# Kernel optimization log

Hardware: AMD Instinct MI355X
Metric: run time of the kernel (lower is better)

Reference implementation:

```python
import jax, jax.numpy as jnp
import numpy as np

B, M, D = 16, 100000, 128
OUT = 128  # out_features; in_features = 2*D


def setup_inputs() -> dict:
    key = jax.random.key(0)
    k1, k2, k3, k4 = jax.random.split(key, 4)
    s1 = 1.0 / np.sqrt(2 * D)  # ~ torch Linear default init scale
    s2 = 1.0 / np.sqrt(OUT)
    return {
        "xx_anchor": jax.random.normal(k1, (B, D), dtype=jnp.float32),
        "input": jax.random.normal(k2, (M, D), dtype=jnp.float32),
        "adj": jnp.zeros((1, 1), dtype=jnp.float32),  # densified then unused in forward math
        "W1": jax.random.normal(k3, (OUT, 2 * D), dtype=jnp.float32) * s1,
        "W2": jax.random.normal(k4, (1, OUT), dtype=jnp.float32) * s2,
    }


def reference(xx_anchor, input, adj, W1, W2):
    d = input.shape[1]
    # concat(q_vec, input) @ W1.T  ==  q @ W1[:, :d].T  +  input @ W1[:, d:].T
    # (avoids materializing the [B, m, 2d] concat tensor; same math)
    anchor_part = xx_anchor @ W1[:, :d].T          # [B, out]
    node_part = input @ W1[:, d:].T                # [m, out]
    h = jax.nn.relu(anchor_part[:, None, :] + node_part[None, :, :])  # [B, m, out]
    scores = jnp.einsum('bmo,o->bm', h, W2[0])     # linear2 -> [B, m]
    atten = jax.nn.softmax(scores, axis=1)          # softmax over node dim
    v_vec = jnp.einsum('bm,md->bd', atten, input)   # weighted sum pooling
    return v_vec
```

## Files before the change

### kernel.cpp

```cpp
#include <hip/hip_runtime.h>
#include <hip/hip_bf16.h>
#include <math.h>


typedef __attribute__((ext_vector_type(8))) short bf16x8;
typedef __attribute__((ext_vector_type(4))) float f32x4;

__device__ __forceinline__ short f2bs(float f) {
    __hip_bfloat16 h = __float2bfloat16(f);
    return *reinterpret_cast<short*>(&h);
}
__device__ __forceinline__ float bs2f(ushort u) {
    union { unsigned int i; float f; } v; v.i = ((unsigned)u) << 16; return v.f;
}

__global__ __launch_bounds__(256) void kA(const float* __restrict__ W1,
                                          const float* __restrict__ xx,
                                          ushort* __restrict__ w1b,
                                          float* __restrict__ A) {
    const int bi = blockIdx.x, t = threadIdx.x;
    if (bi < 64) {
        int idx = bi * 256 + t;
        int o = idx >> 7, d = idx & 127;
        w1b[idx] = (ushort)f2bs(W1[o * 256 + 128 + d]);
        return;
    }
    __shared__ float xxs[16 * 132];
    __shared__ float w1s[16 * 132];
    const int og0 = (bi - 64) * 16;
#pragma unroll
    for (int i = 0; i < 2; ++i) {
        int idx = t + 256 * i;
        int r = idx >> 5, c4 = (idx & 31) << 2;
        *(float4*)&xxs[r * 132 + c4] = *(const float4*)&xx[r * 128 + c4];
        *(float4*)&w1s[r * 132 + c4] = *(const float4*)&W1[(og0 + r) * 256 + c4];
    }
    __syncthreads();
    const int ol = t >> 4, b = t & 15;
    float acc = 0.f;
#pragma unroll
    for (int d4 = 0; d4 < 32; ++d4) {
        float4 xv = *(float4*)&xxs[b * 132 + d4 * 4];
        float4 wv = *(float4*)&w1s[ol * 132 + d4 * 4];
        acc += xv.x * wv.x + xv.y * wv.y + xv.z * wv.z + xv.w * wv.w;
    }
    A[b * 128 + og0 + ol] = acc;
}

__global__ __launch_bounds__(256, 4) void kB(
    const float* __restrict__ in, const ushort* __restrict__ w1b,
    const float* __restrict__ W2, const float* __restrict__ A,
    float* __restrict__ lsum_g, ushort* __restrict__ pacc, int M) {
    __shared__ ushort ins[64 * 136];
    __shared__ float As[16 * 128];
    __shared__ ushort pb[16 * 72];

    const int tid = threadIdx.x, bid = blockIdx.x;
    const int m0 = bid * 64;
    const int w = tid >> 6, lane = tid & 63;
    const int c = lane & 15, q = lane >> 4;
    const int lim = (M - m0 < 64) ? (M - m0) : 64;

#pragma unroll
    for (int i = 0; i < 8; ++i) {
        int idx = tid + 256 * i;
        int r = idx >> 5, c4 = (idx & 31) << 2;
        float4 v = make_float4(0.f, 0.f, 0.f, 0.f);
        if (r < lim) v = *(const float4*)&in[(size_t)(m0 + r) * 128 + c4];
        ushort4 u;
        u.x = (ushort)f2bs(v.x); u.y = (ushort)f2bs(v.y);
        u.z = (ushort)f2bs(v.z); u.w = (ushort)f2bs(v.w);
        *(ushort4*)&ins[r * 136 + c4] = u;
    }
#pragma unroll
    for (int i = 0; i < 8; ++i) {
        int idx = tid + 256 * i;
        As[idx] = A[idx];
    }
    __syncthreads();

    const ushort* mrow = &ins[(w * 16 + c) * 136];
    f32x4 acc[8];
#pragma unroll
    for (int ot = 0; ot < 8; ++ot) acc[ot] = (f32x4){0.f, 0.f, 0.f, 0.f};
#pragma unroll
    for (int kb = 0; kb < 4; ++kb) {
        bf16x8 bv_in = *(const bf16x8*)(mrow + kb * 32 + q * 8);
#pragma unroll
        for (int ot = 0; ot < 8; ++ot) {
            bf16x8 av_w1 = *(const bf16x8*)(w1b + (ot * 16 + c) * 128 + kb * 32 + q * 8);
            acc[ot] = __builtin_amdgcn_mfma_f32_16x16x32_bf16(av_w1, bv_in, acc[ot], 0, 0, 0);
        }
    }

    f32x4 w2q[8];
#pragma unroll
    for (int ot = 0; ot < 8; ++ot)
        w2q[ot] = *(const f32x4*)&W2[ot * 16 + q * 4];

    const bool mvalid = (w * 16 + c) < lim;
#pragma unroll
    for (int b = 0; b < 16; ++b) {
        float s0 = 0.f, s1 = 0.f, s2 = 0.f, s3 = 0.f;
#pragma unroll
        for (int ot = 0; ot < 8; ++ot) {
            f32x4 aq = *(f32x4*)&As[b * 128 + ot * 16 + q * 4];
            s0 += fmaxf(acc[ot][0] + aq[0], 0.f) * w2q[ot][0];
            s1 += fmaxf(acc[ot][1] + aq[1], 0.f) * w2q[ot][1];
            s2 += fmaxf(acc[ot][2] + aq[2], 0.f) * w2q[ot][2];
            s3 += fmaxf(acc[ot][3] + aq[3], 0.f) * w2q[ot][3];
        }
        float sacc = (s0 + s1) + (s2 + s3);
        sacc += __shfl_xor(sacc, 16, 64);
        sacc += __shfl_xor(sacc, 32, 64);
        if (q == (b & 3)) {
            float p = mvalid ? __expf(sacc) : 0.f;
            pb[b * 72 + w * 16 + c] = (ushort)f2bs(p);
        }
    }
    __syncthreads();

    f32x4 pd[2];
    pd[0] = (f32x4){0.f, 0.f, 0.f, 0.f};
    pd[1] = (f32x4){0.f, 0.f, 0.f, 0.f};
#pragma unroll
    for (int s = 0; s < 2; ++s) {
        bf16x8 pf = *(const bf16x8*)(pb + c * 72 + s * 32 + q * 8);
#pragma unroll
        for (int t = 0; t < 2; ++t) {
            const int dloc = w * 32 + t * 16 + c;
            bf16x8 bf;
#pragma unroll
            for (int j = 0; j < 8; ++j)
                bf[j] = (short)ins[(s * 32 + q * 8 + j) * 136 + dloc];
            pd[t] = __builtin_amdgcn_mfma_f32_16x16x32_bf16(pf, bf, pd[t], 0, 0, 0);
        }
    }
#pragma unroll
    for (int t = 0; t < 2; ++t)
#pragma unroll
        for (int r = 0; r < 4; ++r)
            pacc[((size_t)bid * 16 + q * 4 + r) * 128 + w * 32 + t * 16 + c] =
                (ushort)f2bs(pd[t][r]);

    {
        const int b = tid >> 4, jj = tid & 15;
        const ushort* pr = &pb[b * 72 + jj * 4];
        float part = bs2f(pr[0]) + bs2f(pr[1]) + bs2f(pr[2]) + bs2f(pr[3]);
#pragma unroll
        for (int off = 1; off < 16; off <<= 1) part += __shfl_xor(part, off, 64);
        if (jj == 0) lsum_g[bid * 16 + b] = part;
    }
}

__global__ __launch_bounds__(256) void kC1(
    const float* __restrict__ lsum_g, const ushort* __restrict__ pacc,
    float* __restrict__ pacc2, float* __restrict__ lsum2, int nb) {
    const int b = blockIdx.x >> 4, s = blockIdx.x & 15;
    const int t = threadIdx.x;
    __shared__ float reda[2 * 128];
    __shared__ float redl[2];
    const int cs = (nb + 15) >> 4;
    const int blk0 = s * cs;
    int blk1 = blk0 + cs; if (blk1 > nb) blk1 = nb;
    const int dd = t & 127, h = t >> 7;
    float ac = 0.f, ls = 0.f;
    for (int blk = blk0 + h; blk < blk1; blk += 2) {
        ac += bs2f(pacc[((size_t)blk * 16 + b) * 128 + dd]);
        ls += lsum_g[blk * 16 + b];
    }
    reda[h * 128 + dd] = ac;
    if (dd == 0) redl[h] = ls;
    __syncthreads();
    if (h == 0) {
        pacc2[((size_t)s * 16 + b) * 128 + dd] = reda[dd] + reda[128 + dd];
        if (dd == 0) lsum2[s * 16 + b] = redl[0] + redl[1];
    }
}

__global__ void kFin(const float* __restrict__ pacc2, const float* __restrict__ lsum2,
                     float* __restrict__ out) {
    const int b = blockIdx.x, t = threadIdx.x;
    float ac = 0.f, ls = 0.f;
#pragma unroll
    for (int s = 0; s < 16; ++s) {
        ac += pacc2[((size_t)s * 16 + b) * 128 + t];
        ls += lsum2[s * 16 + b];
    }
    out[b * 128 + t] = ac / ls;
}

extern "C" void kernel_launch(void* const* d_in, const int* in_sizes, int n_in,
                              void* d_out, int out_size, void* d_ws, size_t ws_size,
                              hipStream_t stream) {
    const float* xx = (const float*)d_in[0];
    const float* in = (const float*)d_in[1];
    const float* W1 = (const float*)d_in[3];
    const float* W2 = (const float*)d_in[4];
    float* out = (float*)d_out;

    const int M = in_sizes[1] / 128;
    const int nb = (M + 63) / 64;

    float* ws = (float*)d_ws;
    float* A      = ws;
    float* lsum_g = A + 2048;
    float* pacc2  = lsum_g + (size_t)nb * 16;
    float* lsum2  = pacc2 + 256 * 128;
    ushort* w1b   = (ushort*)(lsum2 + 256);
    ushort* pacc  = w1b + 16384;

    kA  <<<72, 256, 0, stream>>>(W1, xx, w1b, A);
    kB  <<<nb, 256, 0, stream>>>(in, w1b, W2, A, lsum_g, pacc, M);
    kC1 <<<256, 256, 0, stream>>>(lsum_g, pacc, pacc2, lsum2, nb);
    kFin<<<16, 128, 0, stream>>>(pacc2, lsum2, out);
}
```

Before: 146.6 us.

## Process 128 nodes per block in kB, reusing W1 fragments across two M tiles

Doubles the node tile per block of the main kernel from 64 to 128 rows, with each wave computing two 16-row MFMA tiles that share each loaded W1 fragment. This halves the global W1 reloads per node and halves the number of blocks, which also halves the partial accumulator rows written to pacc and reduced in kC1. In exchange it uses more registers (two accumulator sets) and more LDS, and lowers the occupancy hint from 4 to 3 blocks per CU. The A load into shared memory is also vectorised to float4.

After: 146.3 us. No clear change (-0.2%).

```diff
diff --git a/kernel.cpp b/kernel.cpp
--- a/kernel.cpp
+++ b/kernel.cpp
@@ -47,22 +47,22 @@
     A[b * 128 + og0 + ol] = acc;
 }
 
-__global__ __launch_bounds__(256, 4) void kB(
+__global__ __launch_bounds__(256, 3) void kB(
     const float* __restrict__ in, const ushort* __restrict__ w1b,
     const float* __restrict__ W2, const float* __restrict__ A,
     float* __restrict__ lsum_g, ushort* __restrict__ pacc, int M) {
-    __shared__ ushort ins[64 * 136];
+    __shared__ ushort ins[128 * 136];
     __shared__ float As[16 * 128];
-    __shared__ ushort pb[16 * 72];
+    __shared__ ushort pb[16 * 136];
 
     const int tid = threadIdx.x, bid = blockIdx.x;
-    const int m0 = bid * 64;
+    const int m0 = bid * 128;
     const int w = tid >> 6, lane = tid & 63;
     const int c = lane & 15, q = lane >> 4;
-    const int lim = (M - m0 < 64) ? (M - m0) : 64;
-
-#pragma unroll
-    for (int i = 0; i < 8; ++i) {
+    const int lim = (M - m0 < 128) ? (M - m0) : 128;
+
+#pragma unroll
+    for (int i = 0; i < 16; ++i) {
         int idx = tid + 256 * i;
         int r = idx >> 5, c4 = (idx & 31) << 2;
         float4 v = make_float4(0.f, 0.f, 0.f, 0.f);
@@ -73,23 +73,27 @@
         *(ushort4*)&ins[r * 136 + c4] = u;
     }
 #pragma unroll
-    for (int i = 0; i < 8; ++i) {
+    for (int i = 0; i < 2; ++i) {
         int idx = tid + 256 * i;
-        As[idx] = A[idx];
-    }
-    __syncthreads();
-
-    const ushort* mrow = &ins[(w * 16 + c) * 136];
-    f32x4 acc[8];
-#pragma unroll
-    for (int ot = 0; ot < 8; ++ot) acc[ot] = (f32x4){0.f, 0.f, 0.f, 0.f};
+        *(float4*)&As[idx * 4] = *(const float4*)&A[idx * 4];
+    }
+    __syncthreads();
+
+    const int mbase = w * 32 + c;
+    f32x4 acc[2][8];
+#pragma unroll
+    for (int mt = 0; mt < 2; ++mt)
+#pragma unroll
+        for (int ot = 0; ot < 8; ++ot) acc[mt][ot] = (f32x4){0.f, 0.f, 0.f, 0.f};
 #pragma unroll
     for (int kb = 0; kb < 4; ++kb) {
-        bf16x8 bv_in = *(const bf16x8*)(mrow + kb * 32 + q * 8);
+        bf16x8 bv0 = *(const bf16x8*)&ins[mbase * 136 + kb * 32 + q * 8];
+        bf16x8 bv1 = *(const bf16x8*)&ins[(mbase + 16) * 136 + kb * 32 + q * 8];
 #pragma unroll
         for (int ot = 0; ot < 8; ++ot) {
-            bf16x8 av_w1 = *(const bf16x8*)(w1b + (ot * 16 + c) * 128 + kb * 32 + q * 8);
-            acc[ot] = __builtin_amdgcn_mfma_f32_16x16x32_bf16(av_w1, bv_in, acc[ot], 0, 0, 0);
+            bf16x8 av = *(const bf16x8*)(w1b + (ot * 16 + c) * 128 + kb * 32 + q * 8);
+            acc[0][ot] = __builtin_amdgcn_mfma_f32_16x16x32_bf16(av, bv0, acc[0][ot], 0, 0, 0);
+            acc[1][ot] = __builtin_amdgcn_mfma_f32_16x16x32_bf16(av, bv1, acc[1][ot], 0, 0, 0);
         }
     }
 
@@ -98,24 +102,27 @@
     for (int ot = 0; ot < 8; ++ot)
         w2q[ot] = *(const f32x4*)&W2[ot * 16 + q * 4];
 
-    const bool mvalid = (w * 16 + c) < lim;
+    const bool mv0 = (w * 32 + c) < lim;
+    const bool mv1 = (w * 32 + 16 + c) < lim;
 #pragma unroll
     for (int b = 0; b < 16; ++b) {
-        float s0 = 0.f, s1 = 0.f, s2 = 0.f, s3 = 0.f;
+        float sa0 = 0.f, sa1 = 0.f;
 #pragma unroll
         for (int ot = 0; ot < 8; ++ot) {
             f32x4 aq = *(f32x4*)&As[b * 128 + ot * 16 + q * 4];
-            s0 += fmaxf(acc[ot][0] + aq[0], 0.f) * w2q[ot][0];
-            s1 += fmaxf(acc[ot][1] + aq[1], 0.f) * w2q[ot][1];
-            s2 += fmaxf(acc[ot][2] + aq[2], 0.f) * w2q[ot][2];
-            s3 += fmaxf(acc[ot][3] + aq[3], 0.f) * w2q[ot][3];
-        }
-        float sacc = (s0 + s1) + (s2 + s3);
-        sacc += __shfl_xor(sacc, 16, 64);
-        sacc += __shfl_xor(sacc, 32, 64);
+#pragma unroll
+            for (int r = 0; r < 4; ++r) {
+                sa0 += fmaxf(acc[0][ot][r] + aq[r], 0.f) * w2q[ot][r];
+                sa1 += fmaxf(acc[1][ot][r] + aq[r], 0.f) * w2q[ot][r];
+            }
+        }
+        sa0 += __shfl_xor(sa0, 16, 64);
+        sa0 += __shfl_xor(sa0, 32, 64);
+        sa1 += __shfl_xor(sa1, 16, 64);
+        sa1 += __shfl_xor(sa1, 32, 64);
         if (q == (b & 3)) {
-            float p = mvalid ? __expf(sacc) : 0.f;
-            pb[b * 72 + w * 16 + c] = (ushort)f2bs(p);
+            pb[b * 136 + w * 32 + c]      = (ushort)f2bs(mv0 ? __expf(sa0) : 0.f);
+            pb[b * 136 + w * 32 + 16 + c] = (ushort)f2bs(mv1 ? __expf(sa1) : 0.f);
         }
     }
     __syncthreads();
@@ -124,15 +131,15 @@
     pd[0] = (f32x4){0.f, 0.f, 0.f, 0.f};
     pd[1] = (f32x4){0.f, 0.f, 0.f, 0.f};
 #pragma unroll
-    for (int s = 0; s < 2; ++s) {
-        bf16x8 pf = *(const bf16x8*)(pb + c * 72 + s * 32 + q * 8);
+    for (int ks = 0; ks < 4; ++ks) {
+        bf16x8 pf = *(const bf16x8*)&pb[c * 136 + ks * 32 + q * 8];
 #pragma unroll
         for (int t = 0; t < 2; ++t) {
             const int dloc = w * 32 + t * 16 + c;
             bf16x8 bf;
 #pragma unroll
             for (int j = 0; j < 8; ++j)
-                bf[j] = (short)ins[(s * 32 + q * 8 + j) * 136 + dloc];
+                bf[j] = (short)ins[(ks * 32 + q * 8 + j) * 136 + dloc];
             pd[t] = __builtin_amdgcn_mfma_f32_16x16x32_bf16(pf, bf, pd[t], 0, 0, 0);
         }
     }
@@ -144,12 +151,14 @@
                 (ushort)f2bs(pd[t][r]);
 
     {
-        const int b = tid >> 4, jj = tid & 15;
-        const ushort* pr = &pb[b * 72 + jj * 4];
-        float part = bs2f(pr[0]) + bs2f(pr[1]) + bs2f(pr[2]) + bs2f(pr[3]);
+        const int bb = tid >> 4, jj = tid & 15;
+        const ushort* pr = &pb[bb * 136 + jj * 8];
+        float part = 0.f;
+#pragma unroll
+        for (int j2 = 0; j2 < 8; ++j2) part += bs2f(pr[j2]);
 #pragma unroll
         for (int off = 1; off < 16; off <<= 1) part += __shfl_xor(part, off, 64);
-        if (jj == 0) lsum_g[bid * 16 + b] = part;
+        if (jj == 0) lsum_g[bid * 16 + bb] = part;
     }
 }
 
@@ -200,7 +209,7 @@
     float* out = (float*)d_out;
 
     const int M = in_sizes[1] / 128;
-    const int nb = (M + 63) / 64;
+    const int nb = (M + 127) / 128;
 
     float* ws = (float*)d_ws;
     float* A      = ws;
```

## Merge reduction kernels into one pass and pack score math into f32x2

Applied to the files above, without the earlier changes.

The two-stage cross-block reduction (kC1 with 256 blocks followed by kFin) becomes a single kC kernel. kC launches one block per batch row, walks over all node blocks and writes the normalized output directly. This removes one launch and the intermediate buffers. The trade-off is parallelism: only 16 blocks now run long serial loops over the partial sums. Separately, kB gets a higher occupancy hint in launch_bounds, loads A into shared memory with float4, and computes the relu/W2 score accumulation with packed 2-wide float vectors.

After: 208.0 us. 1.42x slower.

```diff
diff --git a/kernel.cpp b/kernel.cpp
--- a/kernel.cpp
+++ b/kernel.cpp
@@ -5,6 +5,7 @@
 
 typedef __attribute__((ext_vector_type(8))) short bf16x8;
 typedef __attribute__((ext_vector_type(4))) float f32x4;
+typedef __attribute__((ext_vector_type(2))) float f32x2;
 
 __device__ __forceinline__ short f2bs(float f) {
     __hip_bfloat16 h = __float2bfloat16(f);
@@ -47,7 +48,7 @@
     A[b * 128 + og0 + ol] = acc;
 }
 
-__global__ __launch_bounds__(256, 4) void kB(
+__global__ __launch_bounds__(256, 5) void kB(
     const float* __restrict__ in, const ushort* __restrict__ w1b,
     const float* __restrict__ W2, const float* __restrict__ A,
     float* __restrict__ lsum_g, ushort* __restrict__ pacc, int M) {
@@ -73,9 +74,9 @@
         *(ushort4*)&ins[r * 136 + c4] = u;
     }
 #pragma unroll
-    for (int i = 0; i < 8; ++i) {
+    for (int i = 0; i < 2; ++i) {
         int idx = tid + 256 * i;
-        As[idx] = A[idx];
+        *(float4*)&As[idx * 4] = *(const float4*)&A[idx * 4];
     }
     __syncthreads();
 
@@ -99,24 +100,27 @@
         w2q[ot] = *(const f32x4*)&W2[ot * 16 + q * 4];
 
     const bool mvalid = (w * 16 + c) < lim;
+    const f32x2 zero2 = (f32x2){0.f, 0.f};
 #pragma unroll
     for (int b = 0; b < 16; ++b) {
-        float s0 = 0.f, s1 = 0.f, s2 = 0.f, s3 = 0.f;
+        f32x2 sv0 = zero2, sv1 = zero2;
 #pragma unroll
         for (int ot = 0; ot < 8; ++ot) {
-            f32x4 aq = *(f32x4*)&As[b * 128 + ot * 16 + q * 4];
-            s0 += fmaxf(acc[ot][0] + aq[0], 0.f) * w2q[ot][0];
-            s1 += fmaxf(acc[ot][1] + aq[1], 0.f) * w2q[ot][1];
-            s2 += fmaxf(acc[ot][2] + aq[2], 0.f) * w2q[ot][2];
-            s3 += fmaxf(acc[ot][3] + aq[3], 0.f) * w2q[ot][3];
+            const f32x2* aq = (const f32x2*)&As[b * 128 + ot * 16 + q * 4];
+            f32x2 nlo = __builtin_shufflevector(acc[ot], acc[ot], 0, 1);
+            f32x2 nhi = __builtin_shufflevector(acc[ot], acc[ot], 2, 3);
+            f32x2 wlo = __builtin_shufflevector(w2q[ot], w2q[ot], 0, 1);
+            f32x2 whi = __builtin_shufflevector(w2q[ot], w2q[ot], 2, 3);
+            f32x2 z0 = __builtin_elementwise_max(nlo + aq[0], zero2);
+            f32x2 z1 = __builtin_elementwise_max(nhi + aq[1], zero2);
+            sv0 += z0 * wlo;
+            sv1 += z1 * whi;
         }
-        float sacc = (s0 + s1) + (s2 + s3);
+        float sacc = (sv0[0] + sv0[1]) + (sv1[0] + sv1[1]);
         sacc += __shfl_xor(sacc, 16, 64);
         sacc += __shfl_xor(sacc, 32, 64);
-        if (q == (b & 3)) {
-            float p = mvalid ? __expf(sacc) : 0.f;
-            pb[b * 72 + w * 16 + c] = (ushort)f2bs(p);
-        }
+        if (q == (b & 3))
+            pb[b * 72 + w * 16 + c] = (ushort)f2bs(mvalid ? __expf(sacc) : 0.f);
     }
     __syncthreads();
 
@@ -144,50 +148,33 @@
                 (ushort)f2bs(pd[t][r]);
 
     {
-        const int b = tid >> 4, jj = tid & 15;
-        const ushort* pr = &pb[b * 72 + jj * 4];
+        const int bb = tid >> 4, jj = tid & 15;
+        const ushort* pr = &pb[bb * 72 + jj * 4];
         float part = bs2f(pr[0]) + bs2f(pr[1]) + bs2f(pr[2]) + bs2f(pr[3]);
 #pragma unroll
         for (int off = 1; off < 16; off <<= 1) part += __shfl_xor(part, off, 64);
-        if (jj == 0) lsum_g[bid * 16 + b] = part;
-    }
-}
-
-__global__ __launch_bounds__(256) void kC1(
+        if (jj == 0) lsum_g[bid * 16 + bb] = part;
+    }
+}
+
+__global__ __launch_bounds__(256) void kC(
     const float* __restrict__ lsum_g, const ushort* __restrict__ pacc,
-    float* __restrict__ pacc2, float* __restrict__ lsum2, int nb) {
-    const int b = blockIdx.x >> 4, s = blockIdx.x & 15;
-    const int t = threadIdx.x;
+    float* __restrict__ out, int nb) {
+    const int b = blockIdx.x, t = threadIdx.x;
+    const int dd = t & 127, h = t >> 7;
     __shared__ float reda[2 * 128];
     __shared__ float redl[2];
-    const int cs = (nb + 15) >> 4;
-    const int blk0 = s * cs;
-    int blk1 = blk0 + cs; if (blk1 > nb) blk1 = nb;
-    const int dd = t & 127, h = t >> 7;
     float ac = 0.f, ls = 0.f;
-    for (int blk = blk0 + h; blk < blk1; blk += 2) {
+#pragma unroll 4
+    for (int blk = h; blk < nb; blk += 2) {
         ac += bs2f(pacc[((size_t)blk * 16 + b) * 128 + dd]);
         ls += lsum_g[blk * 16 + b];
     }
     reda[h * 128 + dd] = ac;
     if (dd == 0) redl[h] = ls;
     __syncthreads();
-    if (h == 0) {
-        pacc2[((size_t)s * 16 + b) * 128 + dd] = reda[dd] + reda[128 + dd];
-        if (dd == 0) lsum2[s * 16 + b] = redl[0] + redl[1];
-    }
-}
-
-__global__ void kFin(const float* __restrict__ pacc2, const float* __restrict__ lsum2,
-                     float* __restrict__ out) {
-    const int b = blockIdx.x, t = threadIdx.x;
-    float ac = 0.f, ls = 0.f;
-#pragma unroll
-    for (int s = 0; s < 16; ++s) {
-        ac += pacc2[((size_t)s * 16 + b) * 128 + t];
-        ls += lsum2[s * 16 + b];
-    }
-    out[b * 128 + t] = ac / ls;
+    if (h == 0)
+        out[b * 128 + dd] = (reda[dd] + reda[128 + dd]) / (redl[0] + redl[1]);
 }
 
 extern "C" void kernel_launch(void* const* d_in, const int* in_sizes, int n_in,
@@ -205,13 +192,10 @@
     float* ws = (float*)d_ws;
     float* A      = ws;
     float* lsum_g = A + 2048;
-    float* pacc2  = lsum_g + (size_t)nb * 16;
-    float* lsum2  = pacc2 + 256 * 128;
-    ushort* w1b   = (ushort*)(lsum2 + 256);
+    ushort* w1b   = (ushort*)(lsum_g + (size_t)nb * 16);
     ushort* pacc  = w1b + 16384;
 
-    kA  <<<72, 256, 0, stream>>>(W1, xx, w1b, A);
-    kB  <<<nb, 256, 0, stream>>>(in, w1b, W2, A, lsum_g, pacc, M);
-    kC1 <<<256, 256, 0, stream>>>(lsum_g, pacc, pacc2, lsum2, nb);
-    kFin<<<16, 128, 0, stream>>>(pacc2, lsum2, out);
-}
+    kA <<<72, 256, 0, stream>>>(W1, xx, w1b, A);
+    kB <<<nb, 256, 0, stream>>>(in, w1b, W2, A, lsum_g, pacc, M);
+    kC <<<16, 256, 0, stream>>>(lsum_g, pacc, out, nb);
+}
```
